# Performance work log

Measured on AMD Instinct MI355X. Metric: run time of the kernel, lower is better.

## Reference

```python
import jax, jax.numpy as jnp
import numpy as np

B, S, D, H = 16, 1024, 512, 8
DEPTH = D // H  # 64


def setup_inputs() -> dict:
    key = jax.random.key(0)
    ks = jax.random.split(key, 12)
    std = 1.0 / np.sqrt(D)
    inp = {
        "q": jax.random.normal(ks[0], (B, S, D), dtype=jnp.float32),
        "k": jax.random.normal(ks[1], (B, S, D), dtype=jnp.float32),
        "v": jax.random.normal(ks[2], (B, S, D), dtype=jnp.float32),
        "mask": jax.random.randint(ks[3], (B, 1, 1, S), 0, 2, dtype=jnp.int32),
        "wq_w": jax.random.uniform(ks[4], (D, D), jnp.float32, -std, std),
        "wq_b": jax.random.uniform(ks[5], (D,), jnp.float32, -std, std),
        "wk_w": jax.random.uniform(ks[6], (D, D), jnp.float32, -std, std),
        "wk_b": jax.random.uniform(ks[7], (D,), jnp.float32, -std, std),
        "wv_w": jax.random.uniform(ks[8], (D, D), jnp.float32, -std, std),
        "wv_b": jax.random.uniform(ks[9], (D,), jnp.float32, -std, std),
        "wo_w": jax.random.uniform(ks[10], (D, D), jnp.float32, -std, std),
        "wo_b": jax.random.uniform(ks[11], (D,), jnp.float32, -std, std),
    }
    return inp


def reference(q, k, v, mask, wq_w, wq_b, wk_w, wk_b, wv_w, wv_b, wo_w, wo_b):
    b = q.shape[0]
    # QKV projections (torch Linear: x @ W.T + b), then split heads -> [B,H,S,depth]
    def proj(x, w, bias):
        y = x @ w.T + bias
        return y.reshape(b, -1, H, DEPTH).transpose(0, 2, 1, 3)

    qh, kh, vh = proj(q, wq_w, wq_b), proj(k, wk_w, wk_b), proj(v, wv_w, wv_b)

    # scaled dot-product attention with full [B,H,S,S] scores
    logits = jnp.einsum("bhqd,bhkd->bhqk", qh, kh) / jnp.sqrt(jnp.float32(DEPTH))
    logits = logits + mask.astype(logits.dtype) * -1e9
    # NOTE: original code softmaxes over dim=1 (the head axis) -- reproduced faithfully
    attn = jax.nn.softmax(logits, axis=1)
    ctx = jnp.einsum("bhqk,bhkd->bhqd", attn, vh)

    # merge heads and output projection
    ctx = ctx.transpose(0, 2, 1, 3).reshape(b, -1, D)
    out = ctx @ wo_w.T + wo_b
    return out, attn
```

## Files before the change

kernel.cpp:

```cpp
#include <hip/hip_runtime.h>
#include <hip/hip_bf16.h>
#include <math.h>

typedef __attribute__((ext_vector_type(8))) short short8;
typedef __attribute__((ext_vector_type(4))) float f32x4;
typedef __attribute__((ext_vector_type(4))) unsigned short ushort4_t;

#define MFMA16(a, b, c) __builtin_amdgcn_mfma_f32_16x16x32_bf16((a), (b), (c), 0, 0, 0)

#define GLOAD_LDS16(src, ldsbase)                                                     \
  __builtin_amdgcn_global_load_lds(                                                   \
      (const __attribute__((address_space(1))) void*)(src),                           \
      (__attribute__((address_space(3))) void*)(ldsbase), 16, 0, 0)

static __device__ __forceinline__ unsigned short f2bf(float f) {
  __hip_bfloat16 h = __float2bfloat16(f);
  unsigned short u;
  __builtin_memcpy(&u, &h, 2);
  return u;
}

static __device__ __forceinline__ float bf2f(unsigned short b) {
  union { unsigned u; float f; } v; v.u = ((unsigned)b) << 16;
  return v.f;
}

static __device__ __forceinline__ short8 cvt2v(f32x4 a, f32x4 b) {
  short8 t;
#pragma unroll
  for (int j = 0; j < 4; ++j) t[j] = (short)f2bf(a[j]);
#pragma unroll
  for (int j = 0; j < 4; ++j) t[4 + j] = (short)f2bf(b[j]);
  return t;
}

static __device__ __forceinline__ void lds_barrier() {
  __builtin_amdgcn_sched_barrier(0);
  asm volatile("s_waitcnt lgkmcnt(0)" ::: "memory");
  __builtin_amdgcn_s_barrier();
  __builtin_amdgcn_sched_barrier(0);
}

__global__ __launch_bounds__(256) void cvt_w(
    const float* __restrict__ wq, const float* __restrict__ wk,
    const float* __restrict__ wv, const float* __restrict__ wo,
    unsigned short* __restrict__ wq16, unsigned short* __restrict__ wk16,
    unsigned short* __restrict__ wv16, unsigned short* __restrict__ wo16) {
  const int blk = blockIdx.x;
  const float* src;
  unsigned short* dst;
  size_t base;
  if (blk < 128)      { src = wq; dst = wq16; base = (size_t)blk * 2048; }
  else if (blk < 256) { src = wk; dst = wk16; base = (size_t)(blk - 128) * 2048; }
  else if (blk < 384) { src = wv; dst = wv16; base = (size_t)(blk - 256) * 2048; }
  else                { src = wo; dst = wo16; base = (size_t)(blk - 384) * 2048; }
  const size_t i = base + (size_t)threadIdx.x * 8;
  f32x4 a = *(const f32x4*)(src + i);
  f32x4 b = *(const f32x4*)(src + i + 4);
  *(short8*)(dst + i) = cvt2v(a, b);
}

__global__ __launch_bounds__(256) void proj_qk(
    const float* __restrict__ q, const float* __restrict__ k,
    const unsigned short* __restrict__ wq16, const unsigned short* __restrict__ wk16,
    const float* __restrict__ bq, const float* __restrict__ bk,
    unsigned short* __restrict__ qh, unsigned short* __restrict__ kh) {
  __shared__ unsigned short As[128 * 64], Ws[128 * 64];
  const int z = blockIdx.z;
  const float* A = z == 0 ? q : k;
  const unsigned short* W16 = z == 0 ? wq16 : wk16;
  const float* bias = z == 0 ? bq : bk;
  unsigned short* outp = z == 0 ? qh : kh;

  const int tid = threadIdx.x;
  const int wv_ = tid >> 6, lane = tid & 63;
  const int lr = lane & 15, lg = lane >> 4;
  const int m0 = blockIdx.x * 128, n0 = blockIdx.y * 128;
  const int wm = (wv_ >> 1) * 64, wn = (wv_ & 1) * 64;

  f32x4 acc[4][4] = {};

  for (int k0 = 0; k0 < 512; k0 += 64) {
#pragma unroll
    for (int p = 0; p < 4; ++p) {
      const int row = (p * 4 + wv_) * 8 + (lane >> 3);
      const int col = (lane & 7) * 8;
      GLOAD_LDS16(W16 + (size_t)(n0 + row) * 512 + k0 + col, &Ws[(p * 4 + wv_) * 512]);
    }
    const int row = (tid >> 3), col = (tid & 7) * 8;
#pragma unroll
    for (int p = 0; p < 4; ++p) {
      const float* src = A + (size_t)(m0 + p * 32 + row) * 512 + k0 + col;
      f32x4 a0 = *(const f32x4*)src;
      f32x4 a1 = *(const f32x4*)(src + 4);
      *(short8*)&As[(p * 32 + row) * 64 + col] = cvt2v(a0, a1);
    }
    __syncthreads();

#pragma unroll
    for (int ks = 0; ks < 2; ++ks) {
      short8 af[4], bw[4];
#pragma unroll
      for (int mi = 0; mi < 4; ++mi)
        af[mi] = *(const short8*)&As[(wm + mi * 16 + lr) * 64 + ks * 32 + lg * 8];
#pragma unroll
      for (int ni = 0; ni < 4; ++ni)
        bw[ni] = *(const short8*)&Ws[(wn + ni * 16 + lr) * 64 + ks * 32 + lg * 8];
#pragma unroll
      for (int ni = 0; ni < 4; ++ni)
#pragma unroll
        for (int mi = 0; mi < 4; ++mi)
          acc[ni][mi] = MFMA16(bw[ni], af[mi], acc[ni][mi]);
    }
    __syncthreads();
  }

  const int hI = (n0 + wn) >> 6;
#pragma unroll
  for (int ni = 0; ni < 4; ++ni) {
    const int d0 = ni * 16 + 4 * lg;
    f32x4 bvv = *(const f32x4*)&bias[n0 + wn + d0];
#pragma unroll
    for (int mi = 0; mi < 4; ++mi) {
      const int s = m0 + wm + mi * 16 + lr;
      const int bI = s >> 10, srow = s & 1023;
      size_t addr = ((size_t)(bI * 8 + hI) << 16) + (srow >> 4) * 1024 +
                    (d0 >> 5) * 512 + ((d0 >> 3) & 3) * 128 + lr * 8 + (d0 & 7);
      ushort4_t pk;
#pragma unroll
      for (int r = 0; r < 4; ++r) pk[r] = f2bf(acc[ni][mi][r] + bvv[r]);
      *(ushort4_t*)&outp[addr] = pk;
    }
  }
}

__global__ __launch_bounds__(256) void proj_v(
    const float* __restrict__ v, const unsigned short* __restrict__ wv16,
    const float* __restrict__ bv, unsigned short* __restrict__ vt) {
  __shared__ unsigned short As[128 * 64], Ws[128 * 64];
  const int tid = threadIdx.x;
  const int wv_ = tid >> 6, lane = tid & 63;
  const int lr = lane & 15, lg = lane >> 4;
  const int m0 = blockIdx.x * 128, n0 = blockIdx.y * 128;
  const int wm = (wv_ >> 1) * 64, wn = (wv_ & 1) * 64;

  f32x4 acc[4][4] = {};

  for (int k0 = 0; k0 < 512; k0 += 64) {
#pragma unroll
    for (int p = 0; p < 4; ++p) {
      const int row = (p * 4 + wv_) * 8 + (lane >> 3);
      const int col = (lane & 7) * 8;
      GLOAD_LDS16(wv16 + (size_t)(n0 + row) * 512 + k0 + col, &Ws[(p * 4 + wv_) * 512]);
    }
    const int row = (tid >> 3), col = (tid & 7) * 8;
#pragma unroll
    for (int p = 0; p < 4; ++p) {
      const float* src = v + (size_t)(m0 + p * 32 + row) * 512 + k0 + col;
      f32x4 a0 = *(const f32x4*)src;
      f32x4 a1 = *(const f32x4*)(src + 4);
      *(short8*)&As[(p * 32 + row) * 64 + col] = cvt2v(a0, a1);
    }
    __syncthreads();

#pragma unroll
    for (int ks = 0; ks < 2; ++ks) {
      short8 af[4], bw[4];
#pragma unroll
      for (int mi = 0; mi < 4; ++mi)
        af[mi] = *(const short8*)&As[(wm + mi * 16 + lr) * 64 + ks * 32 + lg * 8];
#pragma unroll
      for (int ni = 0; ni < 4; ++ni)
        bw[ni] = *(const short8*)&Ws[(wn + ni * 16 + lr) * 64 + ks * 32 + lg * 8];
#pragma unroll
      for (int mi = 0; mi < 4; ++mi)
#pragma unroll
        for (int ni = 0; ni < 4; ++ni)
          acc[mi][ni] = MFMA16(af[mi], bw[ni], acc[mi][ni]);
    }
    __syncthreads();
  }

  const int hI = (n0 + wn) >> 6;
#pragma unroll
  for (int ni = 0; ni < 4; ++ni) {
    const float bv_ = bv[n0 + wn + ni * 16 + lr];
#pragma unroll
    for (int mi = 0; mi < 4; ++mi) {
      const int s0 = m0 + wm + mi * 16 + 4 * lg;
      const int bI = s0 >> 10, srow = s0 & 1023;
      size_t addr = ((size_t)(bI * 8 + hI) << 16) + (srow >> 6) * 4096 + ni * 1024 +
                    ((srow >> 5) & 1) * 512 + ((srow >> 3) & 3) * 128 + lr * 8 + (srow & 7);
      ushort4_t pk;
#pragma unroll
      for (int r = 0; r < 4; ++r) pk[r] = f2bf(acc[mi][ni][r] + bv_);
      *(ushort4_t*)&vt[addr] = pk;
    }
  }
}

__global__ __launch_bounds__(256) void out_gemm(const unsigned short* __restrict__ A,
                                                const unsigned short* __restrict__ W16,
                                                const float* __restrict__ bias,
                                                float* __restrict__ out_) {
  __shared__ unsigned short As[128 * 64], Ws[128 * 64];
  const int tid = threadIdx.x;
  const int wv_ = tid >> 6, lane = tid & 63;
  const int lr = lane & 15, lg = lane >> 4;
  const int m0 = blockIdx.x * 128, n0 = blockIdx.y * 128;
  const int wm = (wv_ >> 1) * 64, wn = (wv_ & 1) * 64;

  f32x4 acc[4][4] = {};

  for (int k0 = 0; k0 < 512; k0 += 64) {
#pragma unroll
    for (int p = 0; p < 4; ++p) {
      const int row = (p * 4 + wv_) * 8 + (lane >> 3);
      const int col = (lane & 7) * 8;
      GLOAD_LDS16(A + (size_t)(m0 + row) * 512 + k0 + col, &As[(p * 4 + wv_) * 512]);
      GLOAD_LDS16(W16 + (size_t)(n0 + row) * 512 + k0 + col, &Ws[(p * 4 + wv_) * 512]);
    }
    __syncthreads();

#pragma unroll
    for (int ks = 0; ks < 2; ++ks) {
      short8 af[4], bw[4];
#pragma unroll
      for (int mi = 0; mi < 4; ++mi)
        af[mi] = *(const short8*)&As[(wm + mi * 16 + lr) * 64 + ks * 32 + lg * 8];
#pragma unroll
      for (int ni = 0; ni < 4; ++ni)
        bw[ni] = *(const short8*)&Ws[(wn + ni * 16 + lr) * 64 + ks * 32 + lg * 8];
#pragma unroll
      for (int ni = 0; ni < 4; ++ni)
#pragma unroll
        for (int mi = 0; mi < 4; ++mi)
          acc[ni][mi] = MFMA16(bw[ni], af[mi], acc[ni][mi]);
    }
    __syncthreads();
  }

#pragma unroll
  for (int ni = 0; ni < 4; ++ni) {
    const int c0 = n0 + wn + ni * 16 + 4 * lg;
    f32x4 bvv = *(const f32x4*)&bias[c0];
#pragma unroll
    for (int mi = 0; mi < 4; ++mi) {
      const int rg = m0 + wm + mi * 16 + lr;
      f32x4 val = acc[ni][mi] + bvv;
      *(f32x4*)&out_[(size_t)rg * 512 + c0] = val;
    }
  }
}

__global__ __launch_bounds__(512, 4) void attn_fused(
    const unsigned short* __restrict__ qh, const unsigned short* __restrict__ kh,
    const unsigned short* __restrict__ vt, const int* __restrict__ mask,
    float* __restrict__ attn_out, unsigned short* __restrict__ ctx) {
  __shared__ unsigned short sb[2][8][32][72];
  __shared__ float mf[1024];

  const int tid = threadIdx.x;
  const int h = tid >> 6, lane = tid & 63;
  const int lr = lane & 15, lg = lane >> 4;

  const int lin = blockIdx.x + 32 * blockIdx.y;
  const int xcd = lin & 7, slot = lin >> 3;
  const int b = xcd + 8 * (slot >> 5);
  const int q0 = (slot & 31) * 32;

  const unsigned short* qb = qh + ((size_t)(b * 8 + h) << 16);
  const unsigned short* kb = kh + ((size_t)(b * 8 + h) << 16);
  const unsigned short* vb = vt + ((size_t)(b * 8 + h) << 16);

#pragma unroll
  for (int i = 0; i < 2; ++i)
    mf[tid + i * 512] = -1e9f * (float)mask[b * 1024 + tid + i * 512];

  short8 qf[2][2];
#pragma unroll
  for (int qi = 0; qi < 2; ++qi)
#pragma unroll
    for (int ks = 0; ks < 2; ++ks)
      qf[qi][ks] = *(const short8*)(qb + ((q0 >> 4) + qi) * 1024 + ks * 512 + lane * 8);

  const int sq = tid >> 4, sk4 = tid & 15;

  f32x4 apv[2][4] = {};

  lds_barrier();

  for (int kt = 0; kt < 16; ++kt) {
    const int k0 = kt * 64;
    unsigned short(*sc)[32][72] = sb[kt & 1];

    short8 kf[4][2];
#pragma unroll
    for (int ki = 0; ki < 4; ++ki)
#pragma unroll
      for (int ks = 0; ks < 2; ++ks)
        kf[ki][ks] = *(const short8*)(kb + ((k0 >> 4) + ki) * 1024 + ks * 512 + lane * 8);
    f32x4 aqk[4][2] = {};
#pragma unroll
    for (int ks = 0; ks < 2; ++ks)
#pragma unroll
      for (int ki = 0; ki < 4; ++ki)
#pragma unroll
        for (int qi = 0; qi < 2; ++qi)
          aqk[ki][qi] = MFMA16(kf[ki][ks], qf[qi][ks], aqk[ki][qi]);

#pragma unroll
    for (int ki = 0; ki < 4; ++ki) {
      f32x4 mv = *(const f32x4*)&mf[k0 + ki * 16 + 4 * lg];
#pragma unroll
      for (int qi = 0; qi < 2; ++qi) {
        ushort4_t pk;
#pragma unroll
        for (int r = 0; r < 4; ++r) pk[r] = f2bf(aqk[ki][qi][r] * 0.125f + mv[r]);
        *(ushort4_t*)&sc[h][qi * 16 + lr][ki * 16 + 4 * lg] = pk;
      }
    }

    short8 vf0[4];
#pragma unroll
    for (int ni = 0; ni < 4; ++ni)
      vf0[ni] = *(const short8*)(vb + kt * 4096 + ni * 1024 + lane * 8);

    lds_barrier();

    f32x4 e[8];
#pragma unroll
    for (int hh = 0; hh < 8; ++hh) {
      ushort4_t raw = *(const ushort4_t*)&sc[hh][sq][4 * sk4];
#pragma unroll
      for (int r = 0; r < 4; ++r) e[hh][r] = bf2f(raw[r]);
    }
    f32x4 mx = e[0];
#pragma unroll
    for (int hh = 1; hh < 8; ++hh)
#pragma unroll
      for (int r = 0; r < 4; ++r) mx[r] = fmaxf(mx[r], e[hh][r]);
    f32x4 s = {0.f, 0.f, 0.f, 0.f};
#pragma unroll
    for (int hh = 0; hh < 8; ++hh) {
#pragma unroll
      for (int r = 0; r < 4; ++r) e[hh][r] = __expf(e[hh][r] - mx[r]);
      s += e[hh];
    }
    f32x4 inv;
#pragma unroll
    for (int r = 0; r < 4; ++r) inv[r] = __builtin_amdgcn_rcpf(s[r]);

    float* abase = attn_out + (((size_t)(b * 8) * 1024 + q0 + sq) * 1024) + k0 + 4 * sk4;
#pragma unroll
    for (int hh = 0; hh < 8; ++hh) {
      f32x4 p = e[hh] * inv;
      __builtin_nontemporal_store(p, (f32x4*)(abase + ((size_t)hh << 20)));
      ushort4_t pk;
#pragma unroll
      for (int r = 0; r < 4; ++r) pk[r] = f2bf(p[r]);
      *(ushort4_t*)&sc[hh][sq][4 * sk4] = pk;
    }

    short8 vf1[4];
#pragma unroll
    for (int ni = 0; ni < 4; ++ni)
      vf1[ni] = *(const short8*)(vb + kt * 4096 + ni * 1024 + 512 + lane * 8);

    lds_barrier();

    short8 pf[2][2];
#pragma unroll
    for (int mi = 0; mi < 2; ++mi)
#pragma unroll
      for (int ks = 0; ks < 2; ++ks)
        pf[mi][ks] = *(const short8*)&sc[h][mi * 16 + lr][ks * 32 + 8 * lg];
#pragma unroll
    for (int mi = 0; mi < 2; ++mi)
#pragma unroll
      for (int ni = 0; ni < 4; ++ni)
        apv[mi][ni] = MFMA16(pf[mi][0], vf0[ni], apv[mi][ni]);
#pragma unroll
    for (int mi = 0; mi < 2; ++mi)
#pragma unroll
      for (int ni = 0; ni < 4; ++ni)
        apv[mi][ni] = MFMA16(pf[mi][1], vf1[ni], apv[mi][ni]);
  }

#pragma unroll
  for (int mi = 0; mi < 2; ++mi)
#pragma unroll
    for (int ni = 0; ni < 4; ++ni)
#pragma unroll
      for (int r = 0; r < 4; ++r) {
        const int row = q0 + mi * 16 + 4 * lg + r;
        const int col = h * 64 + ni * 16 + lr;
        ctx[((size_t)b * 1024 + row) * 512 + col] = f2bf(apv[mi][ni][r]);
      }
}

extern "C" void kernel_launch(void* const* d_in, const int* in_sizes, int n_in,
                              void* d_out, int out_size, void* d_ws, size_t ws_size,
                              hipStream_t stream) {
  const float* q = (const float*)d_in[0];
  const float* k = (const float*)d_in[1];
  const float* v = (const float*)d_in[2];
  const int* mask = (const int*)d_in[3];
  const float* wq_w = (const float*)d_in[4];
  const float* wq_b = (const float*)d_in[5];
  const float* wk_w = (const float*)d_in[6];
  const float* wk_b = (const float*)d_in[7];
  const float* wv_w = (const float*)d_in[8];
  const float* wv_b = (const float*)d_in[9];
  const float* wo_w = (const float*)d_in[10];
  const float* wo_b = (const float*)d_in[11];

  float* out = (float*)d_out;
  float* attn = out + (size_t)16 * 1024 * 512;

  unsigned short* wq16 = (unsigned short*)(attn + (134217728 - 393216));
  unsigned short* wk16 = wq16 + 262144;
  unsigned short* wv16 = wk16 + 262144;

  unsigned short* qh = (unsigned short*)d_ws;
  unsigned short* kh = qh + (size_t)16 * 8 * 1024 * 64;
  unsigned short* vt = kh + (size_t)16 * 8 * 1024 * 64;
  unsigned short* ctx = vt + (size_t)16 * 8 * 1024 * 64;
  unsigned short* wo16 = ctx + (size_t)16 * 1024 * 512;

  cvt_w<<<dim3(512), dim3(256), 0, stream>>>(wq_w, wk_w, wv_w, wo_w,
                                             wq16, wk16, wv16, wo16);
  proj_qk<<<dim3(128, 4, 2), dim3(256), 0, stream>>>(q, k, wq16, wk16, wq_b, wk_b, qh, kh);
  proj_v<<<dim3(128, 4), dim3(256), 0, stream>>>(v, wv16, wv_b, vt);
  attn_fused<<<dim3(32, 16), dim3(512), 0, stream>>>(qh, kh, vt, mask, attn, ctx);
  out_gemm<<<dim3(128, 4), dim3(256), 0, stream>>>(ctx, wo16, wo_b, out);
}
```

Before: 225.3 us.

## Fuse output projection into attention kernel and merge QKV projection launches

Drops the separate out_gemm kernel. Each attention block now writes its bf16 context tile to LDS and multiplies it directly by a pre-fragmented bf16 Wo, which cvt_w now lays out in MFMA fragment order. This removes the ctx round trip through global memory and one launch. The Q/K and V projection kernels are also merged into one launch with a z-dimension of 3. In exchange, every attention block re-reads all of Wo from global memory and the attention kernel's tail gets longer, which may add register pressure.

```diff
diff --git a/kernel.cpp b/kernel.cpp
--- a/kernel.cpp
+++ b/kernel.cpp
@@ -50,27 +50,37 @@
   const float* src;
   unsigned short* dst;
   size_t base;
+  bool frag = false;
   if (blk < 128)      { src = wq; dst = wq16; base = (size_t)blk * 2048; }
   else if (blk < 256) { src = wk; dst = wk16; base = (size_t)(blk - 128) * 2048; }
   else if (blk < 384) { src = wv; dst = wv16; base = (size_t)(blk - 256) * 2048; }
-  else                { src = wo; dst = wo16; base = (size_t)(blk - 384) * 2048; }
+  else                { src = wo; dst = wo16; base = (size_t)(blk - 384) * 2048; frag = true; }
   const size_t i = base + (size_t)threadIdx.x * 8;
   f32x4 a = *(const f32x4*)(src + i);
   f32x4 b = *(const f32x4*)(src + i + 4);
-  *(short8*)(dst + i) = cvt2v(a, b);
-}
-
-__global__ __launch_bounds__(256) void proj_qk(
-    const float* __restrict__ q, const float* __restrict__ k,
+  if (!frag) {
+    *(short8*)(dst + i) = cvt2v(a, b);
+  } else {
+    const int c = (int)(i >> 9), k = (int)(i & 511);
+    size_t addr = (size_t)(c >> 4) * 8192 + (k >> 5) * 512 + ((k >> 3) & 3) * 128 +
+                  (c & 15) * 8 + (k & 7);
+    *(short8*)(dst + addr) = cvt2v(a, b);
+  }
+}
+
+__global__ __launch_bounds__(256) void proj_gemm(
+    const float* __restrict__ q, const float* __restrict__ k, const float* __restrict__ v,
     const unsigned short* __restrict__ wq16, const unsigned short* __restrict__ wk16,
-    const float* __restrict__ bq, const float* __restrict__ bk,
-    unsigned short* __restrict__ qh, unsigned short* __restrict__ kh) {
+    const unsigned short* __restrict__ wv16,
+    const float* __restrict__ bq, const float* __restrict__ bk, const float* __restrict__ bv,
+    unsigned short* __restrict__ qh, unsigned short* __restrict__ kh,
+    unsigned short* __restrict__ vt) {
   __shared__ unsigned short As[128 * 64], Ws[128 * 64];
   const int z = blockIdx.z;
-  const float* A = z == 0 ? q : k;
-  const unsigned short* W16 = z == 0 ? wq16 : wk16;
-  const float* bias = z == 0 ? bq : bk;
-  unsigned short* outp = z == 0 ? qh : kh;
+  const float* A = z == 0 ? q : z == 1 ? k : v;
+  const unsigned short* W16 = z == 0 ? wq16 : z == 1 ? wk16 : wv16;
+  const float* bias = z == 0 ? bq : z == 1 ? bk : bv;
+  unsigned short* outp = z == 0 ? qh : z == 1 ? kh : vt;
 
   const int tid = threadIdx.x;
   const int wv_ = tid >> 6, lane = tid & 63;
@@ -106,149 +116,56 @@
 #pragma unroll
       for (int ni = 0; ni < 4; ++ni)
         bw[ni] = *(const short8*)&Ws[(wn + ni * 16 + lr) * 64 + ks * 32 + lg * 8];
-#pragma unroll
-      for (int ni = 0; ni < 4; ++ni)
+      if (z < 2) {
+#pragma unroll
+        for (int ni = 0; ni < 4; ++ni)
+#pragma unroll
+          for (int mi = 0; mi < 4; ++mi)
+            acc[ni][mi] = MFMA16(bw[ni], af[mi], acc[ni][mi]);
+      } else {
 #pragma unroll
         for (int mi = 0; mi < 4; ++mi)
-          acc[ni][mi] = MFMA16(bw[ni], af[mi], acc[ni][mi]);
+#pragma unroll
+          for (int ni = 0; ni < 4; ++ni)
+            acc[mi][ni] = MFMA16(af[mi], bw[ni], acc[mi][ni]);
+      }
     }
     __syncthreads();
   }
 
   const int hI = (n0 + wn) >> 6;
-#pragma unroll
-  for (int ni = 0; ni < 4; ++ni) {
-    const int d0 = ni * 16 + 4 * lg;
-    f32x4 bvv = *(const f32x4*)&bias[n0 + wn + d0];
-#pragma unroll
-    for (int mi = 0; mi < 4; ++mi) {
-      const int s = m0 + wm + mi * 16 + lr;
-      const int bI = s >> 10, srow = s & 1023;
-      size_t addr = ((size_t)(bI * 8 + hI) << 16) + (srow >> 4) * 1024 +
-                    (d0 >> 5) * 512 + ((d0 >> 3) & 3) * 128 + lr * 8 + (d0 & 7);
-      ushort4_t pk;
-#pragma unroll
-      for (int r = 0; r < 4; ++r) pk[r] = f2bf(acc[ni][mi][r] + bvv[r]);
-      *(ushort4_t*)&outp[addr] = pk;
-    }
-  }
-}
-
-__global__ __launch_bounds__(256) void proj_v(
-    const float* __restrict__ v, const unsigned short* __restrict__ wv16,
-    const float* __restrict__ bv, unsigned short* __restrict__ vt) {
-  __shared__ unsigned short As[128 * 64], Ws[128 * 64];
-  const int tid = threadIdx.x;
-  const int wv_ = tid >> 6, lane = tid & 63;
-  const int lr = lane & 15, lg = lane >> 4;
-  const int m0 = blockIdx.x * 128, n0 = blockIdx.y * 128;
-  const int wm = (wv_ >> 1) * 64, wn = (wv_ & 1) * 64;
-
-  f32x4 acc[4][4] = {};
-
-  for (int k0 = 0; k0 < 512; k0 += 64) {
-#pragma unroll
-    for (int p = 0; p < 4; ++p) {
-      const int row = (p * 4 + wv_) * 8 + (lane >> 3);
-      const int col = (lane & 7) * 8;
-      GLOAD_LDS16(wv16 + (size_t)(n0 + row) * 512 + k0 + col, &Ws[(p * 4 + wv_) * 512]);
-    }
-    const int row = (tid >> 3), col = (tid & 7) * 8;
-#pragma unroll
-    for (int p = 0; p < 4; ++p) {
-      const float* src = v + (size_t)(m0 + p * 32 + row) * 512 + k0 + col;
-      f32x4 a0 = *(const f32x4*)src;
-      f32x4 a1 = *(const f32x4*)(src + 4);
-      *(short8*)&As[(p * 32 + row) * 64 + col] = cvt2v(a0, a1);
-    }
-    __syncthreads();
-
-#pragma unroll
-    for (int ks = 0; ks < 2; ++ks) {
-      short8 af[4], bw[4];
-#pragma unroll
-      for (int mi = 0; mi < 4; ++mi)
-        af[mi] = *(const short8*)&As[(wm + mi * 16 + lr) * 64 + ks * 32 + lg * 8];
-#pragma unroll
-      for (int ni = 0; ni < 4; ++ni)
-        bw[ni] = *(const short8*)&Ws[(wn + ni * 16 + lr) * 64 + ks * 32 + lg * 8];
-#pragma unroll
-      for (int mi = 0; mi < 4; ++mi)
-#pragma unroll
-        for (int ni = 0; ni < 4; ++ni)
-          acc[mi][ni] = MFMA16(af[mi], bw[ni], acc[mi][ni]);
-    }
-    __syncthreads();
-  }
-
-  const int hI = (n0 + wn) >> 6;
-#pragma unroll
-  for (int ni = 0; ni < 4; ++ni) {
-    const float bv_ = bv[n0 + wn + ni * 16 + lr];
-#pragma unroll
-    for (int mi = 0; mi < 4; ++mi) {
-      const int s0 = m0 + wm + mi * 16 + 4 * lg;
-      const int bI = s0 >> 10, srow = s0 & 1023;
-      size_t addr = ((size_t)(bI * 8 + hI) << 16) + (srow >> 6) * 4096 + ni * 1024 +
-                    ((srow >> 5) & 1) * 512 + ((srow >> 3) & 3) * 128 + lr * 8 + (srow & 7);
-      ushort4_t pk;
-#pragma unroll
-      for (int r = 0; r < 4; ++r) pk[r] = f2bf(acc[mi][ni][r] + bv_);
-      *(ushort4_t*)&vt[addr] = pk;
-    }
-  }
-}
-
-__global__ __launch_bounds__(256) void out_gemm(const unsigned short* __restrict__ A,
-                                                const unsigned short* __restrict__ W16,
-                                                const float* __restrict__ bias,
-                                                float* __restrict__ out_) {
-  __shared__ unsigned short As[128 * 64], Ws[128 * 64];
-  const int tid = threadIdx.x;
-  const int wv_ = tid >> 6, lane = tid & 63;
-  const int lr = lane & 15, lg = lane >> 4;
-  const int m0 = blockIdx.x * 128, n0 = blockIdx.y * 128;
-  const int wm = (wv_ >> 1) * 64, wn = (wv_ & 1) * 64;
-
-  f32x4 acc[4][4] = {};
-
-  for (int k0 = 0; k0 < 512; k0 += 64) {
-#pragma unroll
-    for (int p = 0; p < 4; ++p) {
-      const int row = (p * 4 + wv_) * 8 + (lane >> 3);
-      const int col = (lane & 7) * 8;
-      GLOAD_LDS16(A + (size_t)(m0 + row) * 512 + k0 + col, &As[(p * 4 + wv_) * 512]);
-      GLOAD_LDS16(W16 + (size_t)(n0 + row) * 512 + k0 + col, &Ws[(p * 4 + wv_) * 512]);
-    }
-    __syncthreads();
-
-#pragma unroll
-    for (int ks = 0; ks < 2; ++ks) {
-      short8 af[4], bw[4];
-#pragma unroll
-      for (int mi = 0; mi < 4; ++mi)
-        af[mi] = *(const short8*)&As[(wm + mi * 16 + lr) * 64 + ks * 32 + lg * 8];
-#pragma unroll
-      for (int ni = 0; ni < 4; ++ni)
-        bw[ni] = *(const short8*)&Ws[(wn + ni * 16 + lr) * 64 + ks * 32 + lg * 8];
-#pragma unroll
-      for (int ni = 0; ni < 4; ++ni)
-#pragma unroll
-        for (int mi = 0; mi < 4; ++mi)
-          acc[ni][mi] = MFMA16(bw[ni], af[mi], acc[ni][mi]);
-    }
-    __syncthreads();
-  }
-
-#pragma unroll
-  for (int ni = 0; ni < 4; ++ni) {
-    const int c0 = n0 + wn + ni * 16 + 4 * lg;
-    f32x4 bvv = *(const f32x4*)&bias[c0];
-#pragma unroll
-    for (int mi = 0; mi < 4; ++mi) {
-      const int rg = m0 + wm + mi * 16 + lr;
-      f32x4 val = acc[ni][mi] + bvv;
-      *(f32x4*)&out_[(size_t)rg * 512 + c0] = val;
+  if (z < 2) {
+#pragma unroll
+    for (int ni = 0; ni < 4; ++ni) {
+      const int d0 = ni * 16 + 4 * lg;
+      f32x4 bvv = *(const f32x4*)&bias[n0 + wn + d0];
+#pragma unroll
+      for (int mi = 0; mi < 4; ++mi) {
+        const int s = m0 + wm + mi * 16 + lr;
+        const int bI = s >> 10, srow = s & 1023;
+        size_t addr = ((size_t)(bI * 8 + hI) << 16) + (srow >> 4) * 1024 +
+                      (d0 >> 5) * 512 + ((d0 >> 3) & 3) * 128 + lr * 8 + (d0 & 7);
+        ushort4_t pk;
+#pragma unroll
+        for (int r = 0; r < 4; ++r) pk[r] = f2bf(acc[ni][mi][r] + bvv[r]);
+        *(ushort4_t*)&outp[addr] = pk;
+      }
+    }
+  } else {
+#pragma unroll
+    for (int ni = 0; ni < 4; ++ni) {
+      const float bv_ = bias[n0 + wn + ni * 16 + lr];
+#pragma unroll
+      for (int mi = 0; mi < 4; ++mi) {
+        const int s0 = m0 + wm + mi * 16 + 4 * lg;
+        const int bI = s0 >> 10, srow = s0 & 1023;
+        size_t addr = ((size_t)(bI * 8 + hI) << 16) + (srow >> 6) * 4096 + ni * 1024 +
+                      ((srow >> 5) & 1) * 512 + ((srow >> 3) & 3) * 128 + lr * 8 + (srow & 7);
+        ushort4_t pk;
+#pragma unroll
+        for (int r = 0; r < 4; ++r) pk[r] = f2bf(acc[mi][ni][r] + bv_);
+        *(ushort4_t*)&vt[addr] = pk;
+      }
     }
   }
 }
@@ -256,7 +173,8 @@
 __global__ __launch_bounds__(512, 4) void attn_fused(
     const unsigned short* __restrict__ qh, const unsigned short* __restrict__ kh,
     const unsigned short* __restrict__ vt, const int* __restrict__ mask,
-    float* __restrict__ attn_out, unsigned short* __restrict__ ctx) {
+    const unsigned short* __restrict__ wo16, const float* __restrict__ wo_b,
+    float* __restrict__ attn_out, float* __restrict__ out) {
   __shared__ unsigned short sb[2][8][32][72];
   __shared__ float mf[1024];
 
@@ -387,16 +305,48 @@
         apv[mi][ni] = MFMA16(pf[mi][1], vf1[ni], apv[mi][ni]);
   }
 
+  unsigned short* ctxs = &sb[0][0][0][0];
 #pragma unroll
   for (int mi = 0; mi < 2; ++mi)
 #pragma unroll
     for (int ni = 0; ni < 4; ++ni)
 #pragma unroll
       for (int r = 0; r < 4; ++r) {
-        const int row = q0 + mi * 16 + 4 * lg + r;
+        const int row = mi * 16 + 4 * lg + r;
         const int col = h * 64 + ni * 16 + lr;
-        ctx[((size_t)b * 1024 + row) * 512 + col] = f2bf(apv[mi][ni][r]);
-      }
+        ctxs[row * 520 + col] = f2bf(apv[mi][ni][r]);
+      }
+  lds_barrier();
+
+  f32x4 acc2[4][2] = {};
+#pragma unroll 4
+  for (int ks = 0; ks < 16; ++ks) {
+    short8 ctxf[2];
+#pragma unroll
+    for (int mi2 = 0; mi2 < 2; ++mi2)
+      ctxf[mi2] = *(const short8*)&ctxs[(mi2 * 16 + lr) * 520 + ks * 32 + lg * 8];
+    short8 wof[4];
+#pragma unroll
+    for (int ni2 = 0; ni2 < 4; ++ni2)
+      wof[ni2] = *(const short8*)(wo16 + (size_t)(h * 4 + ni2) * 8192 + ks * 512 + lane * 8);
+#pragma unroll
+    for (int ni2 = 0; ni2 < 4; ++ni2)
+#pragma unroll
+      for (int mi2 = 0; mi2 < 2; ++mi2)
+        acc2[ni2][mi2] = MFMA16(wof[ni2], ctxf[mi2], acc2[ni2][mi2]);
+  }
+
+#pragma unroll
+  for (int ni2 = 0; ni2 < 4; ++ni2) {
+    const int c0 = h * 64 + ni2 * 16 + 4 * lg;
+    f32x4 bvv = *(const f32x4*)&wo_b[c0];
+#pragma unroll
+    for (int mi2 = 0; mi2 < 2; ++mi2) {
+      const int rg = b * 1024 + q0 + mi2 * 16 + lr;
+      f32x4 val = acc2[ni2][mi2] + bvv;
+      *(f32x4*)&out[(size_t)rg * 512 + c0] = val;
+    }
+  }
 }
 
 extern "C" void kernel_launch(void* const* d_in, const int* in_sizes, int n_in,
@@ -425,13 +375,12 @@
   unsigned short* qh = (unsigned short*)d_ws;
   unsigned short* kh = qh + (size_t)16 * 8 * 1024 * 64;
   unsigned short* vt = kh + (size_t)16 * 8 * 1024 * 64;
-  unsigned short* ctx = vt + (size_t)16 * 8 * 1024 * 64;
-  unsigned short* wo16 = ctx + (size_t)16 * 1024 * 512;
+  unsigned short* wo16 = vt + (size_t)16 * 8 * 1024 * 64;
 
   cvt_w<<<dim3(512), dim3(256), 0, stream>>>(wq_w, wk_w, wv_w, wo_w,
                                              wq16, wk16, wv16, wo16);
-  proj_qk<<<dim3(128, 4, 2), dim3(256), 0, stream>>>(q, k, wq16, wk16, wq_b, wk_b, qh, kh);
-  proj_v<<<dim3(128, 4), dim3(256), 0, stream>>>(v, wv16, wv_b, vt);
-  attn_fused<<<dim3(32, 16), dim3(512), 0, stream>>>(qh, kh, vt, mask, attn, ctx);
-  out_gemm<<<dim3(128, 4), dim3(256), 0, stream>>>(ctx, wo16, wo_b, out);
-}
+  proj_gemm<<<dim3(128, 4, 3), dim3(256), 0, stream>>>(
+      q, k, v, wq16, wk16, wv16, wq_b, wk_b, wv_b, qh, kh, vt);
+  attn_fused<<<dim3(32, 16), dim3(512), 0, stream>>>(qh, kh, vt, mask, wo16, wo_b,
+                                                     attn, out);
+}
```

After: 213.4 us (median of 2 runs). 1.06x faster.
